# Kernel optimization log

Measured on AMD Instinct MI355X. Metric: run time of the kernel, lower is better.

The kernel has to match this reference:

```python
import jax, jax.numpy as jnp
import numpy as np
from jax import lax

B, S, D, H = 64, 512, 768, 1024

def setup_inputs() -> dict:
    key = jax.random.key(0)
    ks = jax.random.split(key, 11)
    s = 0.02
    return {
        "x":  jax.random.normal(ks[0], (B, S, D), jnp.float32),
        "Wm": jax.random.normal(ks[1], (H, D), jnp.float32) * s,  # markov: 768->1024
        "bm": jnp.zeros((H,), jnp.float32),
        "Wh": jax.random.normal(ks[2], (H, D), jnp.float32) * s,  # hc1: 768->1024
        "bh": jnp.zeros((H,), jnp.float32),
        "Wz": jax.random.normal(ks[3], (H, 2 * H), jnp.float32) * s,  # update gate
        "bz": jnp.zeros((H,), jnp.float32),
        "Wr": jax.random.normal(ks[4], (H, 2 * H), jnp.float32) * s,  # reset gate
        "br": jnp.zeros((H,), jnp.float32),
        "Wi": jax.random.normal(ks[5], (H, 2 * H), jnp.float32) * s,  # candidate gate
        "bi": jnp.zeros((H,), jnp.float32),
    }


def reference(x, Wm, bm, Wh, bh, Wz, bz, Wr, br, Wi, bi):
    # initial hidden = hc1(first token), shape [B, H]
    h0 = x[:, 0, :] @ Wh.T + bh
    # markov projection batched over all timesteps: [B, S, H]
    u = jnp.einsum("bsd,hd->bsh", x, Wm) + bm

    def step(h, u_t):  # h: [B,H], u_t: [B,H]
        comb = jnp.concatenate([u_t, h], axis=-1)          # [B, 2H]
        z = jax.nn.sigmoid(comb @ Wz.T + bz)
        r = jax.nn.sigmoid(comb @ Wr.T + br)
        comb_r = jnp.concatenate([u_t, r * h], axis=-1)    # [B, 2H]
        h_prime = jnp.tanh(comb_r @ Wi.T + bi)
        h_new = (1.0 - z) * h + z * h_prime
        return h_new, None

    h_final, _ = lax.scan(step, h0, jnp.swapaxes(u, 0, 1))  # scan over S
    return h_final[:, None, :]  # [B, 1, H]
```

## Files before the change

kernel.cpp:

```cpp
#include <hip/hip_runtime.h>
#include <hip/hip_bf16.h>
#include <stdint.h>


#define B_  64
#define S_  512
#define D_  768
#define H_  1024

typedef __attribute__((ext_vector_type(8))) short short8;
typedef __attribute__((ext_vector_type(4))) float f32x4;

static __device__ __forceinline__ short f2bf(float f) {
  union { float f; uint32_t u; } v; v.f = f;
  uint32_t u = v.u;
  u += 0x7FFFu + ((u >> 16) & 1u);
  return (short)(u >> 16);
}
static __device__ __forceinline__ float bf2f(short s) {
  union { uint32_t u; float f; } v; v.u = ((uint32_t)(uint16_t)s) << 16;
  return v.f;
}
static __device__ __forceinline__ void load_lds16(const void* g, void* l) {
  __builtin_amdgcn_global_load_lds((const __attribute__((address_space(1))) void*)g,
                                   (__attribute__((address_space(3))) void*)l, 16, 0, 0);
}

static __device__ __forceinline__ short8 load_frag_sys(const short* p) {
  short8 v;
  asm volatile("global_load_dwordx4 %0, %1, off sc0 sc1" : "=v"(v) : "v"(p));
  return v;
}
static __device__ __forceinline__ void store_bf16_sys(short* p, uint32_t v) {
  asm volatile("global_store_short %0, %1, off sc0 sc1" :: "v"(p), "v"(v) : "memory");
}
static __device__ __forceinline__ void store_flag(uint32_t* p, uint32_t v) {
  asm volatile("global_store_dword %0, %1, off sc0 sc1" :: "v"(p), "v"(v) : "memory");
}
static __device__ __forceinline__ void wait_vm0() {
  asm volatile("s_waitcnt vmcnt(0)" ::: "memory");
  __builtin_amdgcn_sched_barrier(0);
}
static __device__ __forceinline__ void poll16(const uint32_t* base, uint32_t target) {
  const uint32_t* addr = base + ((threadIdx.x & 15) << 4);
  for (;;) {
    uint32_t v;
    asm volatile("global_load_dword %0, %1, off sc0 sc1\n\ts_waitcnt vmcnt(0)"
                 : "=v"(v) : "v"(addr) : "memory");
    if (__all((int)(v >= target))) break;
    __builtin_amdgcn_s_sleep(1);
  }
  __builtin_amdgcn_sched_barrier(0);
}


__global__ void cast_f32_bf16_kernel(const float* __restrict__ in, short* __restrict__ out, int n8) {
  int i = blockIdx.x * blockDim.x + threadIdx.x;
  int stride = gridDim.x * blockDim.x;
  for (; i < n8; i += stride) {
    const f32x4* p = (const f32x4*)(in + (size_t)i * 8);
    f32x4 a = p[0], b = p[1];
    short8 o;
    o[0] = f2bf(a[0]); o[1] = f2bf(a[1]); o[2] = f2bf(a[2]); o[3] = f2bf(a[3]);
    o[4] = f2bf(b[0]); o[5] = f2bf(b[1]); o[6] = f2bf(b[2]); o[7] = f2bf(b[3]);
    *(short8*)(out + (size_t)i * 8) = o;
  }
}

__global__ void build_wcat_kernel(const float* __restrict__ Wz, const float* __restrict__ Wr,
                                  const float* __restrict__ Wi, short* __restrict__ out) {
  int idx = blockIdx.x * blockDim.x + threadIdx.x;
  int n = idx >> 7;
  int k8 = (idx & 127) << 3;
  const float* src;
  if (n < 1024)       src = Wz + ((size_t)n << 11);
  else if (n < 2048)  src = Wr + ((size_t)(n - 1024) << 11);
  else                src = Wi + ((size_t)(n - 2048) << 11);
  const f32x4* p = (const f32x4*)(src + k8);
  f32x4 a = p[0], b = p[1];
  short8 o;
  o[0] = f2bf(a[0]); o[1] = f2bf(a[1]); o[2] = f2bf(a[2]); o[3] = f2bf(a[3]);
  o[4] = f2bf(b[0]); o[5] = f2bf(b[1]); o[6] = f2bf(b[2]); o[7] = f2bf(b[3]);
  *(short8*)(out + ((size_t)n << 10) + k8) = o;
}

__global__ void transpose_cast_kernel(const float* __restrict__ in, short* __restrict__ out) {
  __shared__ float tile[32][33];
  int x = (blockIdx.x << 5) + threadIdx.x;
  int y0 = (blockIdx.y << 5);
#pragma unroll
  for (int i = threadIdx.y; i < 32; i += 8)
    tile[i][threadIdx.x] = in[(size_t)(y0 + i) * 768 + x];
  __syncthreads();
  int ox = (blockIdx.y << 5) + threadIdx.x;
  int oy0 = (blockIdx.x << 5);
#pragma unroll
  for (int i = threadIdx.y; i < 32; i += 8)
    out[(size_t)(oy0 + i) * 1024 + ox] = f2bf(tile[threadIdx.x][i]);
}

__global__ void ccat_kernel(const float* __restrict__ Wz, const float* __restrict__ Wr,
                            const float* __restrict__ Wi, const float* __restrict__ bm,
                            const float* __restrict__ bz, const float* __restrict__ br,
                            const float* __restrict__ bi, float* __restrict__ ccat) {
  int w = (blockIdx.x * blockDim.x + threadIdx.x) >> 6;
  int lane = threadIdx.x & 63;
  if (w >= 3072) return;
  const float* src; const float* bsrc; int ln;
  if (w < 1024)      { src = Wz + ((size_t)w << 11);          bsrc = bz; ln = w; }
  else if (w < 2048) { src = Wr + ((size_t)(w - 1024) << 11); bsrc = br; ln = w - 1024; }
  else               { src = Wi + ((size_t)(w - 2048) << 11); bsrc = bi; ln = w - 2048; }
  float acc = 0.f;
  for (int k = lane; k < 1024; k += 64) acc += src[k] * bm[k];
  for (int off = 32; off > 0; off >>= 1) acc += __shfl_down(acc, off, 64);
  if (lane == 0) ccat[w] = acc + bsrc[ln];
}

__global__ void pack_w_kernel(const float* __restrict__ Wz, const float* __restrict__ Wr,
                              const float* __restrict__ Wi, short* __restrict__ out) {
  int idx = blockIdx.x * blockDim.x + threadIdx.x;
  int lane = idx & 63;
  int t8 = (idx >> 6) & 7;
  int w = (idx >> 9) & 3;
  int j = (idx >> 11) & 63;
  int m = idx >> 17;
  int colv = (j << 4) + (lane & 15);
  int k = 1024 + (w << 8) + (t8 << 5) + ((lane >> 4) << 3);
  const float* W = (m == 0) ? Wr : (m == 1) ? Wz : Wi;
  const float* p = W + ((size_t)colv << 11) + k;
  short8 o;
#pragma unroll
  for (int e = 0; e < 8; ++e) o[e] = f2bf(p[e]);
  *(short8*)(out + ((size_t)idx << 3)) = o;
}


template<bool OUT_F32>
__launch_bounds__(256, 2)
__global__ void gemm_nt_kernel(const short* __restrict__ A, long lda,
                               const short* __restrict__ Bm,
                               void* __restrict__ Cv, int ldc,
                               const float* __restrict__ bias,
                               int M, int N, int K) {
  __shared__ short ldsA[128 * 64];
  __shared__ short ldsB[128 * 64];
  const int tile_m = blockIdx.x << 7;
  const int tile_n = blockIdx.y << 7;
  const int tid = threadIdx.x;
  const int wave = tid >> 6;
  const int lane = tid & 63;
  const int wm = wave & 1;
  const int wn = wave >> 1;
  const int lrow = lane & 15;
  const int lgrp = lane >> 4;

  f32x4 acc[4][4];
#pragma unroll
  for (int a = 0; a < 4; ++a)
#pragma unroll
    for (int b = 0; b < 4; ++b) acc[a][b] = (f32x4){0.f, 0.f, 0.f, 0.f};

  for (int kt = 0; kt < K; kt += 64) {
    __syncthreads();
#pragma unroll
    for (int c = 0; c < 4; ++c) {
      int o = ((wave * 4 + c) << 10) + (lane << 4);
      int row = o >> 7;
      int cb = (o & 127) ^ ((row & 7) << 4);
      int grow = tile_m + row; if (grow >= M) grow = M - 1;
      load_lds16(A + (size_t)grow * lda + kt + (cb >> 1),
                 (char*)ldsA + ((wave * 4 + c) << 10));
      int gcol = tile_n + row;
      load_lds16(Bm + (size_t)gcol * K + kt + (cb >> 1),
                 (char*)ldsB + ((wave * 4 + c) << 10));
    }
    __syncthreads();
#pragma unroll
    for (int kk = 0; kk < 2; ++kk) {
      short8 af[4], bfr[4];
      int kb = (kk << 6) + (lgrp << 4);
#pragma unroll
      for (int a = 0; a < 4; ++a) {
        int r = (wm << 6) + (a << 4) + lrow;
        af[a] = *(const short8*)((const char*)ldsA + (r << 7) + (kb ^ ((r & 7) << 4)));
        int rn = (wn << 6) + (a << 4) + lrow;
        bfr[a] = *(const short8*)((const char*)ldsB + (rn << 7) + (kb ^ ((rn & 7) << 4)));
      }
#pragma unroll
      for (int a = 0; a < 4; ++a)
#pragma unroll
        for (int b = 0; b < 4; ++b)
          acc[a][b] = __builtin_amdgcn_mfma_f32_16x16x32_bf16(af[a], bfr[b], acc[a][b], 0, 0, 0);
    }
  }
#pragma unroll
  for (int a = 0; a < 4; ++a)
#pragma unroll
    for (int b = 0; b < 4; ++b)
#pragma unroll
      for (int q = 0; q < 4; ++q) {
        int r = tile_m + (wm << 6) + (a << 4) + lgrp * 4 + q;
        int cc = tile_n + (wn << 6) + (b << 4) + lrow;
        if (r < M) {
          float v = acc[a][b][q];
          if (bias) v += bias[cc];
          if (OUT_F32) ((float*)Cv)[(size_t)r * ldc + cc] = v;
          else         ((short*)Cv)[(size_t)r * ldc + cc] = f2bf(v);
        }
      }
}


__launch_bounds__(256, 1)
__global__ void recurrence_kernel(const short* __restrict__ pk,
                                  const short* __restrict__ Gcat,
                                  const float* __restrict__ hf,
                                  short* __restrict__ hbf,
                                  short* __restrict__ rhbf,
                                  uint32_t* __restrict__ flags,
                                  float* __restrict__ out) {
  __shared__ float red[3][3][256];
  const int blk = blockIdx.x;
  const int g = blk >> 6;
  const int j = blk & 63;
  const int tid = threadIdx.x;
  const int wave = tid >> 6;
  const int lane = tid & 63;
  const int lrow = lane & 15;
  const int lgrp = lane >> 4;
  const int m0 = g << 4;

  short8 wr[8], wz[8], wi[8];
  {
    const short8* p8 = (const short8*)pk;
    size_t base = ((size_t)j * 4 + wave) * 8;
#pragma unroll
    for (int t8 = 0; t8 < 8; ++t8) wr[t8] = p8[(base + t8) * 64 + lane];
#pragma unroll
    for (int t8 = 0; t8 < 8; ++t8) wz[t8] = p8[((size_t)2048 + base + t8) * 64 + lane];
#pragma unroll
    for (int t8 = 0; t8 < 8; ++t8) wi[t8] = p8[((size_t)4096 + base + t8) * 64 + lane];
  }

  uint32_t* fgrp  = flags + (g << 11);
  const int col = (j << 4) + lrow;
  float hold[4];
  if (wave == 0) {
#pragma unroll
    for (int q = 0; q < 4; ++q)
      hold[q] = hf[((size_t)(m0 + lgrp * 4 + q) << 10) + col];
  }

  const short* hrow  = hbf  + ((size_t)(m0 + lrow) << 10);
  const short* rhrow = rhbf + ((size_t)(m0 + lrow) << 10);
  const int kq = wave << 8;

  float gz[4], gr[4], gi[4], gzn[4], grn[4], gin[4];
  if (wave == 0) {
#pragma unroll
    for (int q = 0; q < 4; ++q) {
      size_t rbase = ((size_t)(m0 + lgrp * 4 + q) * S_) * 3072;
      gz[q] = bf2f(Gcat[rbase + col]);
      gr[q] = bf2f(Gcat[rbase + 1024 + col]);
      gi[q] = bf2f(Gcat[rbase + 2048 + col]);
    }
  }

  for (int t = 0; t < S_; ++t) {
    if (t > 0) poll16(fgrp + 1024 + (wave << 8), (uint32_t)t);
    short8 hfrag[8];
#pragma unroll
    for (int t8 = 0; t8 < 8; ++t8)
      hfrag[t8] = load_frag_sys(hrow + kq + (t8 << 5) + (lgrp << 3));
    wait_vm0();
    f32x4 accr = (f32x4){0.f,0.f,0.f,0.f}, accz = (f32x4){0.f,0.f,0.f,0.f};
#pragma unroll
    for (int t8 = 0; t8 < 8; ++t8) {
      accr = __builtin_amdgcn_mfma_f32_16x16x32_bf16(hfrag[t8], wr[t8], accr, 0, 0, 0);
      accz = __builtin_amdgcn_mfma_f32_16x16x32_bf16(hfrag[t8], wz[t8], accz, 0, 0, 0);
    }
    if (wave != 0) {
#pragma unroll
      for (int q = 0; q < 4; ++q) {
        red[0][wave - 1][lane * 4 + q] = accr[q];
        red[1][wave - 1][lane * 4 + q] = accz[q];
      }
    }
    __syncthreads();
    f32x4 zt = (f32x4){0.f,0.f,0.f,0.f};
    if (wave == 0) {
#pragma unroll
      for (int q = 0; q < 4; ++q) {
        int li = lane * 4 + q;
        float sr = accr[q] + red[0][0][li] + red[0][1][li] + red[0][2][li] + gr[q];
        float sz = accz[q] + red[1][0][li] + red[1][1][li] + red[1][2][li] + gz[q];
        sr = fminf(fmaxf(sr, -30.f), 30.f);
        sz = fminf(fmaxf(sz, -30.f), 30.f);
        float rv = 1.f / (1.f + __expf(-sr));
        zt[q] = 1.f / (1.f + __expf(-sz));
        store_bf16_sys(rhbf + ((size_t)(m0 + lgrp * 4 + q) << 10) + col,
                       (uint32_t)(uint16_t)f2bf(rv * hold[q]));
      }
      wait_vm0();
      if (lane == 0) store_flag(fgrp + (j << 4), (uint32_t)(t + 1));
      int tn = (t < S_ - 1) ? t + 1 : t;
#pragma unroll
      for (int q = 0; q < 4; ++q) {
        size_t rbase = ((size_t)(m0 + lgrp * 4 + q) * S_ + tn) * 3072;
        gzn[q] = bf2f(Gcat[rbase + col]);
        grn[q] = bf2f(Gcat[rbase + 1024 + col]);
        gin[q] = bf2f(Gcat[rbase + 2048 + col]);
      }
    }
    poll16(fgrp + (wave << 8), (uint32_t)(t + 1));
    short8 rhfrag[8];
#pragma unroll
    for (int t8 = 0; t8 < 8; ++t8)
      rhfrag[t8] = load_frag_sys(rhrow + kq + (t8 << 5) + (lgrp << 3));
    wait_vm0();
    f32x4 acci = (f32x4){0.f,0.f,0.f,0.f};
#pragma unroll
    for (int t8 = 0; t8 < 8; ++t8)
      acci = __builtin_amdgcn_mfma_f32_16x16x32_bf16(rhfrag[t8], wi[t8], acci, 0, 0, 0);
    if (wave != 0) {
#pragma unroll
      for (int q = 0; q < 4; ++q) red[2][wave - 1][lane * 4 + q] = acci[q];
    }
    __syncthreads();
    if (wave == 0) {
#pragma unroll
      for (int q = 0; q < 4; ++q) {
        int li = lane * 4 + q;
        float si = acci[q] + red[2][0][li] + red[2][1][li] + red[2][2][li] + gi[q];
        si = fminf(fmaxf(si, -30.f), 30.f);
        float e2 = __expf(2.f * si);
        float hp = (e2 - 1.f) / (e2 + 1.f);
        float hn = (1.f - zt[q]) * hold[q] + zt[q] * hp;
        hold[q] = hn;
        store_bf16_sys(hbf + ((size_t)(m0 + lgrp * 4 + q) << 10) + col,
                       (uint32_t)(uint16_t)f2bf(hn));
        if (t == S_ - 1) out[((size_t)(m0 + lgrp * 4 + q) << 10) + col] = hn;
      }
      wait_vm0();
      if (lane == 0) store_flag(fgrp + 1024 + (j << 4), (uint32_t)(t + 1));
#pragma unroll
      for (int q = 0; q < 4; ++q) { gz[q] = gzn[q]; gr[q] = grn[q]; gi[q] = gin[q]; }
    }
  }
}


extern "C" void kernel_launch(void* const* d_in, const int* in_sizes, int n_in,
                              void* d_out, int out_size, void* d_ws, size_t ws_size,
                              hipStream_t stream) {
  const float* x  = (const float*)d_in[0];
  const float* Wm = (const float*)d_in[1];
  const float* bm = (const float*)d_in[2];
  const float* Wh = (const float*)d_in[3];
  const float* bh = (const float*)d_in[4];
  const float* Wz = (const float*)d_in[5];
  const float* bz = (const float*)d_in[6];
  const float* Wr = (const float*)d_in[7];
  const float* br = (const float*)d_in[8];
  const float* Wi = (const float*)d_in[9];
  const float* bi = (const float*)d_in[10];

  char* ws = (char*)d_ws;
  size_t off = 0;
  auto alloc = [&](size_t bytes) -> void* {
    void* p = ws + off; off += (bytes + 255) & ~(size_t)255; return p;
  };
  short* xbf   = (short*)alloc((size_t)B_ * S_ * D_ * 2);
  short* Gcat  = (short*)alloc((size_t)B_ * S_ * 3072 * 2);
  short* Mcat  = (short*)alloc((size_t)3072 * 768 * 2);
  short* Wcat  = (short*)alloc((size_t)3072 * 1024 * 2);
  short* WmT   = (short*)alloc((size_t)768 * 1024 * 2);
  short* Whbf  = (short*)alloc((size_t)1024 * 768 * 2);
  short* pk    = (short*)alloc((size_t)3 * 1024 * 1024 * 2);
  float* ccat  = (float*)alloc(3072 * 4);
  float* hf    = (float*)alloc(65536 * 4);
  short* hbf   = (short*)alloc(65536 * 2);
  short* rhbf  = (short*)alloc(65536 * 2);
  uint32_t* flags = (uint32_t*)alloc((size_t)4 * 2048 * 4);
  if (off > ws_size) return;

  hipMemsetAsync(flags, 0, (size_t)4 * 2048 * 4, stream);
  cast_f32_bf16_kernel<<<2048, 256, 0, stream>>>(x, xbf, (B_ * S_ * D_) / 8);
  cast_f32_bf16_kernel<<<384, 256, 0, stream>>>(Wh, Whbf, (1024 * 768) / 8);
  build_wcat_kernel<<<1536, 256, 0, stream>>>(Wz, Wr, Wi, Wcat);
  transpose_cast_kernel<<<dim3(24, 32), dim3(32, 8), 0, stream>>>(Wm, WmT);
  ccat_kernel<<<768, 256, 0, stream>>>(Wz, Wr, Wi, bm, bz, br, bi, ccat);
  pack_w_kernel<<<1536, 256, 0, stream>>>(Wz, Wr, Wi, pk);

  gemm_nt_kernel<false><<<dim3(24, 6), 256, 0, stream>>>(Wcat, 1024, WmT, Mcat, 768,
                                                         nullptr, 3072, 768, 1024);
  gemm_nt_kernel<false><<<dim3(256, 24), 256, 0, stream>>>(xbf, 768, Mcat, Gcat, 3072,
                                                           ccat, 32768, 3072, 768);
  gemm_nt_kernel<true><<<dim3(1, 8), 256, 0, stream>>>(xbf, (long)S_ * D_, Whbf, hf, 1024,
                                                       bh, 64, 1024, 768);
  cast_f32_bf16_kernel<<<32, 256, 0, stream>>>(hf, hbf, 65536 / 8);

  recurrence_kernel<<<256, 256, 0, stream>>>(pk, Gcat, hf, hbf, rhbf, flags,
                                             (float*)d_out);
}
```

Measured before the change: 3.676 ms.

## Tile-pack hidden state buffers and use 64-bit atomic swaps for publishing

New measurement: 2.954 ms (median of 2 runs). 1.24x faster.

```diff
diff --git a/kernel.cpp b/kernel.cpp
--- a/kernel.cpp
+++ b/kernel.cpp
@@ -10,6 +10,7 @@
 
 typedef __attribute__((ext_vector_type(8))) short short8;
 typedef __attribute__((ext_vector_type(4))) float f32x4;
+typedef __attribute__((ext_vector_type(4))) unsigned short u16x4;
 
 static __device__ __forceinline__ short f2bf(float f) {
   union { float f; uint32_t u; } v; v.f = f;
@@ -31,11 +32,11 @@
   asm volatile("global_load_dwordx4 %0, %1, off sc0 sc1" : "=v"(v) : "v"(p));
   return v;
 }
-static __device__ __forceinline__ void store_bf16_sys(short* p, uint32_t v) {
-  asm volatile("global_store_short %0, %1, off sc0 sc1" :: "v"(p), "v"(v) : "memory");
-}
-static __device__ __forceinline__ void store_flag(uint32_t* p, uint32_t v) {
-  asm volatile("global_store_dword %0, %1, off sc0 sc1" :: "v"(p), "v"(v) : "memory");
+static __device__ __forceinline__ void atomic_store64(void* p, uint64_t v) {
+  asm volatile("global_atomic_swap_x2 %0, %1, off" :: "v"(p), "v"(v) : "memory");
+}
+static __device__ __forceinline__ void atomic_store32(uint32_t* p, uint32_t v) {
+  asm volatile("global_atomic_swap %0, %1, off" :: "v"(p), "v"(v) : "memory");
 }
 static __device__ __forceinline__ void wait_vm0() {
   asm volatile("s_waitcnt vmcnt(0)" ::: "memory");
@@ -65,6 +66,12 @@
     o[4] = f2bf(b[0]); o[5] = f2bf(b[1]); o[6] = f2bf(b[2]); o[7] = f2bf(b[3]);
     *(short8*)(out + (size_t)i * 8) = o;
   }
+}
+
+__global__ void pack_h0_kernel(const float* __restrict__ hf, short* __restrict__ hp) {
+  int i = blockIdx.x * blockDim.x + threadIdx.x;
+  int col = i & 15, row = (i >> 4) & 15, j = (i >> 8) & 63, g = i >> 14;
+  hp[i] = f2bf(hf[(size_t)(16 * g + row) * 1024 + j * 16 + col]);
 }
 
 __global__ void build_wcat_kernel(const float* __restrict__ Wz, const float* __restrict__ Wr,
@@ -215,11 +222,11 @@
 __global__ void recurrence_kernel(const short* __restrict__ pk,
                                   const short* __restrict__ Gcat,
                                   const float* __restrict__ hf,
-                                  short* __restrict__ hbf,
-                                  short* __restrict__ rhbf,
+                                  short* __restrict__ hp,
+                                  short* __restrict__ rhp,
                                   uint32_t* __restrict__ flags,
                                   float* __restrict__ out) {
-  __shared__ float red[3][3][256];
+  __shared__ float red[3][4][320];
   const int blk = blockIdx.x;
   const int g = blk >> 6;
   const int j = blk & 63;
@@ -242,27 +249,34 @@
     for (int t8 = 0; t8 < 8; ++t8) wi[t8] = p8[((size_t)4096 + base + t8) * 64 + lane];
   }
 
-  uint32_t* fgrp  = flags + (g << 11);
-  const int col = (j << 4) + lrow;
+  uint32_t* fgrp = flags + (g << 11);
+
+  const int row16 = lane >> 2;
+  const int c4 = (lane & 3) << 2;
   float hold[4];
+  float zv[4];
   if (wave == 0) {
 #pragma unroll
-    for (int q = 0; q < 4; ++q)
-      hold[q] = hf[((size_t)(m0 + lgrp * 4 + q) << 10) + col];
-  }
-
-  const short* hrow  = hbf  + ((size_t)(m0 + lrow) << 10);
-  const short* rhrow = rhbf + ((size_t)(m0 + lrow) << 10);
-  const int kq = wave << 8;
+    for (int c = 0; c < 4; ++c)
+      hold[c] = hf[((size_t)(m0 + row16) << 10) + (j << 4) + c4 + c];
+  }
+
+  const size_t cbase = ((size_t)(g * 64) << 8);
+  const int coff = ((16 * wave + (lgrp >> 1)) << 8) + (lrow << 4) + ((lgrp & 1) << 3);
+
+  short* const prodRh = rhp + ((size_t)(g * 64 + j) << 8) + (row16 << 4) + c4;
+  short* const prodH  = hp  + ((size_t)(g * 64 + j) << 8) + (row16 << 4) + c4;
 
   float gz[4], gr[4], gi[4], gzn[4], grn[4], gin[4];
+  const unsigned short* GcatU = (const unsigned short*)Gcat;
   if (wave == 0) {
-#pragma unroll
-    for (int q = 0; q < 4; ++q) {
-      size_t rbase = ((size_t)(m0 + lgrp * 4 + q) * S_) * 3072;
-      gz[q] = bf2f(Gcat[rbase + col]);
-      gr[q] = bf2f(Gcat[rbase + 1024 + col]);
-      gi[q] = bf2f(Gcat[rbase + 2048 + col]);
+    size_t rbase = ((size_t)(m0 + row16) * S_) * 3072 + (j << 4) + c4;
+    u16x4 vz = *(const u16x4*)(GcatU + rbase);
+    u16x4 vr = *(const u16x4*)(GcatU + rbase + 1024);
+    u16x4 vi = *(const u16x4*)(GcatU + rbase + 2048);
+#pragma unroll
+    for (int c = 0; c < 4; ++c) {
+      gz[c] = bf2f((short)vz[c]); gr[c] = bf2f((short)vr[c]); gi[c] = bf2f((short)vi[c]);
     }
   }
 
@@ -271,7 +285,7 @@
     short8 hfrag[8];
 #pragma unroll
     for (int t8 = 0; t8 < 8; ++t8)
-      hfrag[t8] = load_frag_sys(hrow + kq + (t8 << 5) + (lgrp << 3));
+      hfrag[t8] = load_frag_sys(hp + cbase + coff + (t8 << 9));
     wait_vm0();
     f32x4 accr = (f32x4){0.f,0.f,0.f,0.f}, accz = (f32x4){0.f,0.f,0.f,0.f};
 #pragma unroll
@@ -279,72 +293,75 @@
       accr = __builtin_amdgcn_mfma_f32_16x16x32_bf16(hfrag[t8], wr[t8], accr, 0, 0, 0);
       accz = __builtin_amdgcn_mfma_f32_16x16x32_bf16(hfrag[t8], wz[t8], accz, 0, 0, 0);
     }
-    if (wave != 0) {
-#pragma unroll
-      for (int q = 0; q < 4; ++q) {
-        red[0][wave - 1][lane * 4 + q] = accr[q];
-        red[1][wave - 1][lane * 4 + q] = accz[q];
-      }
+#pragma unroll
+    for (int q = 0; q < 4; ++q) {
+      red[0][wave][lane * 5 + q] = accr[q];
+      red[1][wave][lane * 5 + q] = accz[q];
     }
     __syncthreads();
-    f32x4 zt = (f32x4){0.f,0.f,0.f,0.f};
     if (wave == 0) {
-#pragma unroll
-      for (int q = 0; q < 4; ++q) {
-        int li = lane * 4 + q;
-        float sr = accr[q] + red[0][0][li] + red[0][1][li] + red[0][2][li] + gr[q];
-        float sz = accz[q] + red[1][0][li] + red[1][1][li] + red[1][2][li] + gz[q];
+      uint32_t packed[2] = {0u, 0u};
+#pragma unroll
+      for (int c = 0; c < 4; ++c) {
+        int li = (((row16 >> 2) << 4) + c4 + c) * 5 + (row16 & 3);
+        float sr = red[0][0][li] + red[0][1][li] + red[0][2][li] + red[0][3][li] + gr[c];
+        float sz = red[1][0][li] + red[1][1][li] + red[1][2][li] + red[1][3][li] + gz[c];
         sr = fminf(fmaxf(sr, -30.f), 30.f);
         sz = fminf(fmaxf(sz, -30.f), 30.f);
         float rv = 1.f / (1.f + __expf(-sr));
-        zt[q] = 1.f / (1.f + __expf(-sz));
-        store_bf16_sys(rhbf + ((size_t)(m0 + lgrp * 4 + q) << 10) + col,
-                       (uint32_t)(uint16_t)f2bf(rv * hold[q]));
-      }
+        zv[c] = 1.f / (1.f + __expf(-sz));
+        packed[c >> 1] |= ((uint32_t)(uint16_t)f2bf(rv * hold[c])) << ((c & 1) * 16);
+      }
+      atomic_store64(prodRh, ((uint64_t)packed[1] << 32) | packed[0]);
       wait_vm0();
-      if (lane == 0) store_flag(fgrp + (j << 4), (uint32_t)(t + 1));
+      if (lane == 0) atomic_store32(fgrp + (j << 4), (uint32_t)(t + 1));
       int tn = (t < S_ - 1) ? t + 1 : t;
-#pragma unroll
-      for (int q = 0; q < 4; ++q) {
-        size_t rbase = ((size_t)(m0 + lgrp * 4 + q) * S_ + tn) * 3072;
-        gzn[q] = bf2f(Gcat[rbase + col]);
-        grn[q] = bf2f(Gcat[rbase + 1024 + col]);
-        gin[q] = bf2f(Gcat[rbase + 2048 + col]);
+      size_t rbase = ((size_t)(m0 + row16) * S_ + tn) * 3072 + (j << 4) + c4;
+      u16x4 vz = *(const u16x4*)(GcatU + rbase);
+      u16x4 vr = *(const u16x4*)(GcatU + rbase + 1024);
+      u16x4 vi = *(const u16x4*)(GcatU + rbase + 2048);
+#pragma unroll
+      for (int c = 0; c < 4; ++c) {
+        gzn[c] = bf2f((short)vz[c]); grn[c] = bf2f((short)vr[c]); gin[c] = bf2f((short)vi[c]);
       }
     }
     poll16(fgrp + (wave << 8), (uint32_t)(t + 1));
     short8 rhfrag[8];
 #pragma unroll
     for (int t8 = 0; t8 < 8; ++t8)
-      rhfrag[t8] = load_frag_sys(rhrow + kq + (t8 << 5) + (lgrp << 3));
+      rhfrag[t8] = load_frag_sys(rhp + cbase + coff + (t8 << 9));
     wait_vm0();
     f32x4 acci = (f32x4){0.f,0.f,0.f,0.f};
 #pragma unroll
     for (int t8 = 0; t8 < 8; ++t8)
       acci = __builtin_amdgcn_mfma_f32_16x16x32_bf16(rhfrag[t8], wi[t8], acci, 0, 0, 0);
-    if (wave != 0) {
-#pragma unroll
-      for (int q = 0; q < 4; ++q) red[2][wave - 1][lane * 4 + q] = acci[q];
-    }
+#pragma unroll
+    for (int q = 0; q < 4; ++q) red[2][wave][lane * 5 + q] = acci[q];
     __syncthreads();
     if (wave == 0) {
-#pragma unroll
-      for (int q = 0; q < 4; ++q) {
-        int li = lane * 4 + q;
-        float si = acci[q] + red[2][0][li] + red[2][1][li] + red[2][2][li] + gi[q];
+      uint32_t packed[2] = {0u, 0u};
+      float hn4[4];
+#pragma unroll
+      for (int c = 0; c < 4; ++c) {
+        int li = (((row16 >> 2) << 4) + c4 + c) * 5 + (row16 & 3);
+        float si = red[2][0][li] + red[2][1][li] + red[2][2][li] + red[2][3][li] + gi[c];
         si = fminf(fmaxf(si, -30.f), 30.f);
         float e2 = __expf(2.f * si);
-        float hp = (e2 - 1.f) / (e2 + 1.f);
-        float hn = (1.f - zt[q]) * hold[q] + zt[q] * hp;
-        hold[q] = hn;
-        store_bf16_sys(hbf + ((size_t)(m0 + lgrp * 4 + q) << 10) + col,
-                       (uint32_t)(uint16_t)f2bf(hn));
-        if (t == S_ - 1) out[((size_t)(m0 + lgrp * 4 + q) << 10) + col] = hn;
+        float hp_ = (e2 - 1.f) / (e2 + 1.f);
+        float hn = (1.f - zv[c]) * hold[c] + zv[c] * hp_;
+        hold[c] = hn; hn4[c] = hn;
+        packed[c >> 1] |= ((uint32_t)(uint16_t)f2bf(hn)) << ((c & 1) * 16);
+      }
+      atomic_store64(prodH, ((uint64_t)packed[1] << 32) | packed[0]);
+      if (t == S_ - 1) {
+#pragma unroll
+        for (int c = 0; c < 4; ++c)
+          out[((size_t)(m0 + row16) << 10) + (j << 4) + c4 + c] = hn4[c];
       }
       wait_vm0();
-      if (lane == 0) store_flag(fgrp + 1024 + (j << 4), (uint32_t)(t + 1));
-#pragma unroll
-      for (int q = 0; q < 4; ++q) { gz[q] = gzn[q]; gr[q] = grn[q]; gi[q] = gin[q]; }
+      if (lane == 0) atomic_store32(fgrp + 1024 + (j << 4), (uint32_t)(t + 1));
+#pragma unroll
+      for (int c = 0; c < 4; ++c) { gz[c] = gzn[c]; gr[c] = grn[c]; gi[c] = gin[c]; }
     }
   }
 }
@@ -379,8 +396,8 @@
   short* pk    = (short*)alloc((size_t)3 * 1024 * 1024 * 2);
   float* ccat  = (float*)alloc(3072 * 4);
   float* hf    = (float*)alloc(65536 * 4);
-  short* hbf   = (short*)alloc(65536 * 2);
-  short* rhbf  = (short*)alloc(65536 * 2);
+  short* hp    = (short*)alloc(65536 * 2);
+  short* rhp   = (short*)alloc(65536 * 2);
   uint32_t* flags = (uint32_t*)alloc((size_t)4 * 2048 * 4);
   if (off > ws_size) return;
 
@@ -398,8 +415,8 @@
                                                            ccat, 32768, 3072, 768);
   gemm_nt_kernel<true><<<dim3(1, 8), 256, 0, stream>>>(xbf, (long)S_ * D_, Whbf, hf, 1024,
                                                        bh, 64, 1024, 768);
-  cast_f32_bf16_kernel<<<32, 256, 0, stream>>>(hf, hbf, 65536 / 8);
-
-  recurrence_kernel<<<256, 256, 0, stream>>>(pk, Gcat, hf, hbf, rhbf, flags,
+  pack_h0_kernel<<<256, 256, 0, stream>>>(hf, hp);
+
+  recurrence_kernel<<<256, 256, 0, stream>>>(pk, Gcat, hf, hp, rhp, flags,
                                              (float*)d_out);
 }
```
